# Kernel optimization log

Hardware: AMD Instinct MI355X
Metric: run time of the kernel (lower is better)

The kernel has to match this reference:

```python
import jax, jax.numpy as jnp
import numpy as np

E, B, S, C, N, D, DFF, H, K_FREQ = 4, 16, 256, 17, 16, 32, 64, 4, 4
DH = D // H
MA_KERNELS = (4, 8, 12)


def setup_inputs() -> dict:
    key = jax.random.key(0)
    ks = jax.random.split(key, 16)
    sc = 1.0 / np.sqrt(D).astype(np.float32)
    inp = {
        "x": jax.random.normal(ks[0], (B, S, C, 1), jnp.float32),
        "original_x": jax.random.uniform(ks[1], (B, S, 2), jnp.float32),
        "start_W": jax.random.normal(ks[2], (D,), jnp.float32),
        "start_b": jnp.zeros((D,), jnp.float32),
        "Wq": jax.random.normal(ks[3], (E, D, D), jnp.float32) * sc,
        "Wk": jax.random.normal(ks[4], (E, D, D), jnp.float32) * sc,
        "Wv": jax.random.normal(ks[5], (E, D, D), jnp.float32) * sc,
        "Wo": jax.random.normal(ks[6], (E, D, D), jnp.float32) * sc,
        "ln1_g": jnp.ones((E, D), jnp.float32),
        "ln1_b": jnp.zeros((E, D), jnp.float32),
        "ln2_g": jnp.ones((E, D), jnp.float32),
        "ln2_b": jnp.zeros((E, D), jnp.float32),
        "W1": jax.random.normal(ks[7], (E, D, DFF), jnp.float32) * sc,
        "b1": jnp.zeros((E, DFF), jnp.float32),
        "W2": jax.random.normal(ks[8], (E, DFF, D), jnp.float32) * (1.0 / np.sqrt(DFF).astype(np.float32)),
        "b2": jnp.zeros((E, D), jnp.float32),
    }
    return inp


def _moving_avg(x, k):
    # x: [B,S,Ch], replicate-pad then uniform window of size k (stride 1)
    front = jnp.repeat(x[:, :1], (k - 1) // 2, axis=1)
    end = jnp.repeat(x[:, -1:], k // 2, axis=1)
    xp = jnp.concatenate([front, x, end], axis=1)  # [B, S+k-1, Ch]
    c = jnp.cumsum(xp, axis=1)
    c = jnp.concatenate([jnp.zeros_like(c[:, :1]), c], axis=1)
    return (c[:, k:] - c[:, :-k]) / jnp.asarray(k, x.dtype)


def _fourier_season(x, k):
    # ETSformer-style FourierLayer: keep top-k amplitude frequencies (excluding DC)
    s = x.shape[1]
    xf = jnp.fft.rfft(x, axis=1)            # [B,F,Ch] complex
    amp = jnp.abs(xf)
    amp = amp.at[:, 0, :].set(-jnp.inf)     # exclude DC
    topv = jax.lax.top_k(jnp.moveaxis(amp, 1, -1), k)[0]  # [B,Ch,k]
    thresh = topv[..., -1]                  # [B,Ch]
    mask = amp >= thresh[:, None, :]
    xf_m = jnp.where(mask, xf, 0)
    return jnp.fft.irfft(xf_m, n=s, axis=1).astype(x.dtype)


def _ln(z, g, b):
    m = jnp.mean(z, -1, keepdims=True)
    v = jnp.var(z, -1, keepdims=True)
    return (z - m) * jax.lax.rsqrt(v + 1e-5) * g + b


def _expert_fwd(args):
    h, wq, wk, wv, wo, g1, bg1, g2, bg2, w1, b1e, w2, b2e = args
    # h: [B,S,N,D]; pre-LN MHA over the sequence axis per (batch, node)
    z = _ln(h, g1, bg1)
    q = jnp.einsum('bsnd,de->bsne', z, wq).reshape(B, S, N, H, DH)
    k_ = jnp.einsum('bsnd,de->bsne', z, wk).reshape(B, S, N, H, DH)
    v_ = jnp.einsum('bsnd,de->bsne', z, wv).reshape(B, S, N, H, DH)
    att = jnp.einsum('bqnhd,bknhd->bnhqk', q, k_) * (1.0 / np.sqrt(DH).astype(np.float32))
    att = jax.nn.softmax(att, axis=-1)
    o = jnp.einsum('bnhqk,bknhd->bqnhd', att, v_).reshape(B, S, N, D)
    h = h + jnp.einsum('bsnd,de->bsne', o, wo)
    z2 = _ln(h, g2, bg2)
    f = jax.nn.relu(jnp.einsum('bsnd,df->bsnf', z2, w1) + b1e)
    h = h + jnp.einsum('bsnf,fd->bsnd', f, w2) + b2e
    return h


def reference(x, original_x, start_W, start_b, Wq, Wk, Wv, Wo,
              ln1_g, ln1_b, ln2_g, ln2_b, W1, b1, W2, b2):
    xc = x[:, :, :, 0]                                  # [B,S,C]
    trend = sum(_moving_avg(xc, k) for k in MA_KERNELS) / float(len(MA_KERNELS))
    season = _fourier_season(xc, K_FREQ)
    new_x = xc + season + trend                         # [B,S,C]

    scores = original_x[:, :, -1]                       # [B,S]
    bins = jnp.linspace(scores.min(), scores.max(), E + 1)
    assign = jnp.clip(jnp.searchsorted(bins, scores, side='right') - 1, 0, E - 1)  # [B,S] int

    xns = new_x[:, :, :-1]                              # [B,S,N] drop score channel
    onehot = (assign[None] == jnp.arange(E)[:, None, None])          # [E,B,S] bool
    expert_in = xns[None] * onehot[..., None].astype(xns.dtype)      # [E,B,S,N] dense zero-padded dispatch
    hidden = expert_in[..., None] * start_W + start_b                # [E,B,S,N,D] start_linear

    outs = jax.lax.map(_expert_fwd, (hidden, Wq, Wk, Wv, Wo,
                                     ln1_g, ln1_b, ln2_g, ln2_b, W1, b1, W2, b2))  # [E,B,S,N,D]
    combined = jnp.einsum('ebs,ebsnd->bsnd', onehot.astype(outs.dtype), outs)      # one-hot combine
    return combined
```

## Files before the change

### kernel.cpp

```cpp
#include <hip/hip_runtime.h>
#include <hip/hip_fp16.h>
#include <math.h>

#define BB 16
#define SS 256
#define CC 17
#define NCH 16
#define DD 32
#define DFFN 64
#define HH 4
#define DH 8
#define EE 4

#define WS_K0 16
#define WS_V0 144
#define WS_XNS 512
#define WS_SPI (WS_XNS + BB*SS*NCH)
#define WS_WT  (WS_SPI + BB*SS + 64)
#define WS_WL  (WS_WT + 6144)

#define PRE 0.51006977f

typedef __fp16 hv2 __attribute__((ext_vector_type(2)));

__device__ __forceinline__ unsigned pkh2(float a, float b) {
  hv2 r = __builtin_amdgcn_cvt_pkrtz(a, b);
  unsigned u; __builtin_memcpy(&u, &r, 4);
  return u;
}
__device__ __forceinline__ float fd2(unsigned a, unsigned b, float c) {
  hv2 av, bv;
  __builtin_memcpy(&av, &a, 4);
  __builtin_memcpy(&bv, &b, 4);
  return __builtin_amdgcn_fdot2(av, bv, c, false);
}
__device__ __forceinline__ __half2 u2h2(unsigned u) {
  __half2 h; __builtin_memcpy(&h, &u, 4); return h;
}
template<int PAT>
__device__ __forceinline__ unsigned qdpp(unsigned v) {
  return (unsigned)__builtin_amdgcn_mov_dpp((int)v, PAT, 0xF, 0xF, true);
}
template<int PAT>
__device__ __forceinline__ float qdppf(float v) {
  return __uint_as_float(qdpp<PAT>(__float_as_uint(v)));
}

__launch_bounds__(1024)
__global__ void decomp_prep_kernel(const float* __restrict__ x,
                                   const float* __restrict__ ox,
                                   const float* __restrict__ sb,
                                   const float* __restrict__ g1,
                                   const float* __restrict__ bb1,
                                   const float* __restrict__ Wq,
                                   const float* __restrict__ Wk,
                                   const float* __restrict__ Wv,
                                   const float* __restrict__ Wo,
                                   const float* __restrict__ W1,
                                   const float* __restrict__ W2,
                                   float* __restrict__ ws) {
  const int t = threadIdx.x;
  if (blockIdx.x < 256) {
    const int b = blockIdx.x / NCH;
    const int c = blockIdx.x % NCH;
    __shared__ float xs[SS];
    __shared__ float prr[1024], pii[1024];
    __shared__ float amp[129];
    __shared__ float2 YY[129];
    __shared__ float sth;
    if (t < SS) xs[t] = x[(b*SS + t)*CC + c];
    __syncthreads();
    const float TH0 = 0.024543692606170259f;
    {
      const int f = (t & 127) + 1;
      const int chunk = t >> 7;
      const int s0 = chunk * 32;
      const int ph0 = (f * s0) & 255;
      float si, cr; sincosf(TH0*(float)ph0, &si, &cr);
      float s1, c1; sincosf(TH0*(float)f, &s1, &c1);
      float xr = 0.f, xi = 0.f;
      #pragma unroll 4
      for (int k = 0; k < 32; ++k) {
        float xvv = xs[s0 + k];
        xr += xvv * cr;
        xi -= xvv * si;
        float nc = cr*c1 - si*s1;
        si = si*c1 + cr*s1;
        cr = nc;
      }
      prr[t] = xr; pii[t] = xi;
    }
    __syncthreads();
    if (t < 128) {
      float xr = 0.f, xi = 0.f;
      #pragma unroll
      for (int k2 = 0; k2 < 8; ++k2) { xr += prr[t + 128*k2]; xi += pii[t + 128*k2]; }
      prr[t] = xr; pii[t] = xi;
      amp[t+1] = sqrtf(xr*xr + xi*xi);
    }
    __syncthreads();
    if (t < 64) {
      float a0 = amp[t+1], a1 = amp[t+65];
      int i0 = t+1, i1 = t+65;
      float th = -1e30f;
      for (int r = 0; r < 4; ++r) {
        float mv = (a0 > a1) ? a0 : a1;
        int   mi = (a0 > a1) ? i0 : i1;
        for (int off = 32; off > 0; off >>= 1) {
          float ov = __shfl_xor(mv, off);
          int   oi = __shfl_xor(mi, off);
          if (ov > mv || (ov == mv && oi < mi)) { mv = ov; mi = oi; }
        }
        th = mv;
        if (mi == i0) a0 = -1e30f;
        if (mi == i1) a1 = -1e30f;
      }
      if (t == 0) sth = th;
    }
    __syncthreads();
    if (t < 128) {
      const int f = t + 1;
      float wgt = (amp[f] >= sth) ? ((f == 128) ? 1.0f : 2.0f) * (1.0f/256.0f) : 0.0f;
      YY[f] = make_float2(wgt * prr[t], wgt * pii[t]);
    }
    __syncthreads();
    {
      const int s = t & 255;
      const int fc = t >> 8;
      const int f0 = 1 + fc*32;
      const int ph0 = (s * f0) & 255;
      float si, cr; sincosf(TH0*(float)ph0, &si, &cr);
      float s1, c1; sincosf(TH0*(float)s, &s1, &c1);
      float acc = 0.f;
      #pragma unroll 4
      for (int k = 0; k < 32; ++k) {
        float2 y = YY[f0 + k];
        acc += y.x*cr - y.y*si;
        float nc = cr*c1 - si*s1;
        si = si*c1 + cr*s1;
        cr = nc;
      }
      prr[t] = acc;
    }
    __syncthreads();
    if (t < 256) {
      float season = prr[t] + prr[t+256] + prr[t+512] + prr[t+768];
      float s4 = 0.f, s8 = 0.f, s12 = 0.f;
      #pragma unroll
      for (int j = 0; j < 4; ++j)  { int p = t + j - 1; p = p < 0 ? 0 : (p > SS-1 ? SS-1 : p); s4  += xs[p]; }
      #pragma unroll
      for (int j = 0; j < 8; ++j)  { int p = t + j - 3; p = p < 0 ? 0 : (p > SS-1 ? SS-1 : p); s8  += xs[p]; }
      #pragma unroll
      for (int j = 0; j < 12; ++j) { int p = t + j - 5; p = p < 0 ? 0 : (p > SS-1 ? SS-1 : p); s12 += xs[p]; }
      float trend = (s4 * 0.25f + s8 * 0.125f + s12 * (1.0f/12.0f)) * (1.0f/3.0f);
      ws[WS_XNS + (b*SS + t)*NCH + c] = xs[t] + season + trend;
    }
  } else if (blockIdx.x < 272) {
    const int b = blockIdx.x - 256;
    __shared__ float red[32];
    __shared__ int asg[SS];
    __shared__ int cnt[EE];
    __shared__ float z0[EE*DD];
    float mn = 3e38f, mx = -3e38f;
    #pragma unroll
    for (int k = 0; k < 4; ++k) {
      float v = ox[(t + k*1024)*2 + 1];
      mn = fminf(mn, v); mx = fmaxf(mx, v);
    }
    for (int off = 32; off > 0; off >>= 1) {
      mn = fminf(mn, __shfl_xor(mn, off));
      mx = fmaxf(mx, __shfl_xor(mx, off));
    }
    if ((t & 63) == 0) { red[(t>>6)*2] = mn; red[(t>>6)*2+1] = mx; }
    __syncthreads();
    mn = red[0]; mx = red[1];
    #pragma unroll
    for (int w = 1; w < 16; ++w) { mn = fminf(mn, red[w*2]); mx = fmaxf(mx, red[w*2+1]); }
    const float step = (mx - mn) * 0.25f;
    const float e1 = mn + step, e2 = mn + 2.f*step, e3 = mn + 3.f*step;
    if (t < 256) {
      float sc = ox[(b*SS + t)*2 + 1];
      asg[t] = (sc >= e1) + (sc >= e2) + (sc >= e3);
    }
    __syncthreads();
    if (t < EE) {
      int c = 0;
      for (int s2 = 0; s2 < SS; ++s2) c += (asg[s2] == t);
      cnt[t] = c;
    }
    __syncthreads();
    int* SPw  = (int*)ws + WS_SPI;
    int* OFFw = SPw + BB*SS;
    if (t < EE) {
      int off = 0;
      for (int i = 0; i < t; ++i) off += cnt[i];
      OFFw[b*EE + t] = off;
      int kp = off;
      for (int s2 = 0; s2 < SS; ++s2) if (asg[s2] == t) SPw[b*SS + (kp++)] = s2;
    }
    if (t < 128) {
      int ee = t >> 5, d = t & 31;
      float m = 0.f;
      for (int i = 0; i < DD; ++i) m += sb[i];
      m *= (1.0f/DD);
      float var = 0.f;
      for (int i = 0; i < DD; ++i) { float df = sb[i]-m; var += df*df; }
      var *= (1.0f/DD);
      float rs = rsqrtf(var + 1e-5f);
      z0[ee*DD + d] = (sb[d]-m)*rs*g1[ee*DD+d] + bb1[ee*DD+d];
    }
    __syncthreads();
    if (b == 0 && t < 128) {
      int ee = t >> 5, d = t & 31;
      float k0 = 0.f, v0 = 0.f;
      for (int i = 0; i < DD; ++i) {
        float zz = z0[ee*DD + i];
        k0 += zz * Wk[ee*DD*DD + i*DD + d];
        v0 += zz * Wv[ee*DD*DD + i*DD + d];
      }
      ws[WS_K0 + ee*DD + d] = k0;
      ws[WS_V0 + ee*DD + d] = v0;
    }
  } else {
    unsigned* img = (unsigned*)ws + WS_WT;
    const int base_u = (blockIdx.x - 272)*4096;
    #pragma unroll
    for (int i = 0; i < 4; ++i) {
      int u = base_u + i*1024 + t;
      unsigned val;
      if (u < 6144) {
        int mat = u >> 11, r = u & 2047;
        int row = r >> 4, ip = r & 15;
        int e = row >> 5, q = row & 31;
        int d = (q & 3)*8 + (q >> 2);
        const float* Wm = (mat == 0) ? Wq : (mat == 1) ? Wk : Wv;
        const float* src = Wm + e*1024 + d;
        val = pkh2(src[ip*64], src[ip*64 + 32]);
      } else {
        int v = u - 6144;
        if (v < 2048) {
          int row = v >> 4, ip = v & 15;
          int e = row >> 5, q = row & 31;
          int d = (q & 3)*8 + (q >> 2);
          const float* src = Wo + e*1024 + d;
          val = pkh2(src[ip*64], src[ip*64 + 32]);
        } else if (v < 6144) {
          int r = v - 2048;
          int row = r >> 4, ip = r & 15;
          int e = row >> 6, q = row & 63;
          int j = (q & 3)*16 + (q >> 2);
          const float* src = W1 + e*2048 + j;
          val = pkh2(src[ip*128], src[ip*128 + 64]);
        } else {
          int r = v - 6144;
          int a = r >> 11, rr = r & 2047;
          int row = rr >> 4, ip = rr & 15;
          int e = row >> 5, q = row & 31;
          int d = (q & 3)*8 + (q >> 2);
          int jp = a*16 + ip;
          const float* src = W2 + e*2048 + d;
          val = pkh2(src[2*jp*32], src[(2*jp+1)*32]);
        }
      }
      img[u] = val;
    }
  }
}

__launch_bounds__(1024, 4)
__global__ void fused_kernel(const float* __restrict__ ws,
    const float* __restrict__ g1, const float* __restrict__ bb1,
    const float* __restrict__ sW, const float* __restrict__ sb,
    const float* __restrict__ g2, const float* __restrict__ bb2,
    const float* __restrict__ b1, const float* __restrict__ b2,
    float* __restrict__ out) {
  const int blk = blockIdx.x;
  const int n = blk & 15;
  const int b = blk >> 4;
  const int t = threadIdx.x;
  const int p = t >> 2;
  const int hh = t & 3;
  __shared__ unsigned lds[24576];
  unsigned* wT = lds + 8192;
  unsigned* wl = lds + 14336;

  {
    const unsigned* img = (const unsigned*)ws + WS_WT;
    const int wv = t >> 6;
    const int ln = t & 63;
    #pragma unroll
    for (int i = 0; i < 4; ++i) {
      const int ch = wv*4 + i;
      __builtin_amdgcn_global_load_lds(
          (const __attribute__((address_space(1))) unsigned*)(img + ch*256 + ln*4),
          (__attribute__((address_space(3))) unsigned*)(wT + ch*256 + ln*4),
          16, 0, 0);
    }
  }

  const int* SP  = (const int*)ws + WS_SPI;
  const int* OFF = SP + BB*SS;
  const int o1 = OFF[b*4+1], o2v = OFF[b*4+2], o3 = OFF[b*4+3];
  const int e = (p >= o1) + (p >= o2v) + (p >= o3);
  const int beg = (e==0) ? 0  : ((e==1) ? o1 : ((e==2) ? o2v : o3));
  const int end = (e==0) ? o1 : ((e==1) ? o2v : ((e==2) ? o3 : SS));
  const int s = SP[b*SS + p];
  const float xv = ws[WS_XNS + (b*SS + s)*NCH + n];

  float h[DD];
  #pragma unroll
  for (int d = 0; d < DD; ++d) h[d] = xv * sW[d] + sb[d];
  float m = 0.f;
  #pragma unroll
  for (int d = 0; d < DD; ++d) m += h[d];
  m *= (1.0f/DD);
  float var = 0.f;
  #pragma unroll
  for (int d = 0; d < DD; ++d) { float df = h[d]-m; var += df*df; }
  var *= (1.0f/DD);
  float rs = rsqrtf(var + 1e-5f);
  unsigned zp[16];
  #pragma unroll
  for (int ip = 0; ip < 16; ++ip) {
    float za = (h[2*ip]  -m)*rs*g1[e*DD+2*ip]   + bb1[e*DD+2*ip];
    float zb = (h[2*ip+1]-m)*rs*g1[e*DD+2*ip+1] + bb1[e*DD+2*ip+1];
    zp[ip] = pkh2(za, zb);
  }
  __syncthreads();

  float q[DH], kk[DH], vv[DH];
  #pragma unroll
  for (int dd = 0; dd < DH; ++dd) {
    const int row16 = (e*32 + dd*4 + hh)*16;
    const uint4* rq = (const uint4*)&wT[row16];
    const uint4* rk = (const uint4*)&wT[2048 + row16];
    const uint4* rv = (const uint4*)&wT[4096 + row16];
    float aq = 0.f, ak = 0.f, av = 0.f;
    #pragma unroll
    for (int g4 = 0; g4 < 4; ++g4) {
      uint4 wq4 = rq[g4], wk4 = rk[g4], wv4 = rv[g4];
      aq = fd2(zp[4*g4+0], wq4.x, aq); aq = fd2(zp[4*g4+1], wq4.y, aq);
      aq = fd2(zp[4*g4+2], wq4.z, aq); aq = fd2(zp[4*g4+3], wq4.w, aq);
      ak = fd2(zp[4*g4+0], wk4.x, ak); ak = fd2(zp[4*g4+1], wk4.y, ak);
      ak = fd2(zp[4*g4+2], wk4.z, ak); ak = fd2(zp[4*g4+3], wk4.w, ak);
      av = fd2(zp[4*g4+0], wv4.x, av); av = fd2(zp[4*g4+1], wv4.y, av);
      av = fd2(zp[4*g4+2], wv4.z, av); av = fd2(zp[4*g4+3], wv4.w, av);
    }
    q[dd] = aq * PRE; kk[dd] = ak; vv[dd] = av;
  }
  *(uint4*)&lds[p*32 + hh*8]     = make_uint4(pkh2(kk[0],kk[1]), pkh2(kk[2],kk[3]),
                                              pkh2(kk[4],kk[5]), pkh2(kk[6],kk[7]));
  *(uint4*)&lds[p*32 + hh*8 + 4] = make_uint4(pkh2(vv[0],vv[1]), pkh2(vv[2],vv[3]),
                                              pkh2(vv[4],vv[5]), pkh2(vv[6],vv[7]));
  unsigned qp2[4];
  #pragma unroll
  for (int i = 0; i < 4; ++i) qp2[i] = pkh2(q[2*i], q[2*i+1]);
  float s0 = 0.f;
  #pragma unroll
  for (int d = 0; d < DH; ++d) s0 += q[d] * ws[WS_K0 + e*DD + hh*DH + d];
  __syncthreads();

  float wsum = 0.f;
  __half2 o2[4];
  #pragma unroll
  for (int i = 0; i < 4; ++i) o2[i] = u2h2(0u);
  int jk = beg;
  for (; jk + 1 < end; jk += 2) {
    uint4 ku0 = *(const uint4*)&lds[jk*32 + hh*8];
    uint4 vu0 = *(const uint4*)&lds[jk*32 + hh*8 + 4];
    uint4 ku1 = *(const uint4*)&lds[(jk+1)*32 + hh*8];
    uint4 vu1 = *(const uint4*)&lds[(jk+1)*32 + hh*8 + 4];
    float a0 = 0.f, a1 = 0.f;
    a0 = fd2(qp2[0], ku0.x, a0); a0 = fd2(qp2[1], ku0.y, a0);
    a0 = fd2(qp2[2], ku0.z, a0); a0 = fd2(qp2[3], ku0.w, a0);
    a1 = fd2(qp2[0], ku1.x, a1); a1 = fd2(qp2[1], ku1.y, a1);
    a1 = fd2(qp2[2], ku1.z, a1); a1 = fd2(qp2[3], ku1.w, a1);
    float w0f = __builtin_amdgcn_exp2f(a0);
    float w1f = __builtin_amdgcn_exp2f(a1);
    wsum += w0f + w1f;
    __half2 w20 = u2h2(pkh2(w0f, w0f));
    __half2 w21 = u2h2(pkh2(w1f, w1f));
    o2[0] = __hfma2(w20, u2h2(vu0.x), o2[0]);
    o2[1] = __hfma2(w20, u2h2(vu0.y), o2[1]);
    o2[2] = __hfma2(w20, u2h2(vu0.z), o2[2]);
    o2[3] = __hfma2(w20, u2h2(vu0.w), o2[3]);
    o2[0] = __hfma2(w21, u2h2(vu1.x), o2[0]);
    o2[1] = __hfma2(w21, u2h2(vu1.y), o2[1]);
    o2[2] = __hfma2(w21, u2h2(vu1.z), o2[2]);
    o2[3] = __hfma2(w21, u2h2(vu1.w), o2[3]);
  }
  if (jk < end) {
    uint4 ku = *(const uint4*)&lds[jk*32 + hh*8];
    uint4 vu = *(const uint4*)&lds[jk*32 + hh*8 + 4];
    float a = 0.f;
    a = fd2(qp2[0], ku.x, a); a = fd2(qp2[1], ku.y, a);
    a = fd2(qp2[2], ku.z, a); a = fd2(qp2[3], ku.w, a);
    float wf = __builtin_amdgcn_exp2f(a);
    wsum += wf;
    __half2 w2 = u2h2(pkh2(wf, wf));
    o2[0] = __hfma2(w2, u2h2(vu.x), o2[0]);
    o2[1] = __hfma2(w2, u2h2(vu.y), o2[1]);
    o2[2] = __hfma2(w2, u2h2(vu.z), o2[2]);
    o2[3] = __hfma2(w2, u2h2(vu.w), o2[3]);
  }
  float o[DH];
  #pragma unroll
  for (int i = 0; i < 4; ++i) {
    o[2*i]   = __low2float(o2[i]);
    o[2*i+1] = __high2float(o2[i]);
  }
  const int nmis = SS - (end - beg);
  float w0 = (float)nmis * __builtin_amdgcn_exp2f(s0);
  wsum += w0;
  #pragma unroll
  for (int d = 0; d < DH; ++d) o[d] += w0 * ws[WS_V0 + e*DD + hh*DH + d];
  float inv = 1.0f / wsum;
  #pragma unroll
  for (int d = 0; d < DH; ++d) o[d] *= inv;

  unsigned oq[4];
  #pragma unroll
  for (int j = 0; j < 4; ++j) oq[j] = pkh2(o[2*j], o[2*j+1]);
  unsigned ovp[16];
  #pragma unroll
  for (int j = 0; j < 4; ++j) {
    ovp[j]    = qdpp<0x00>(oq[j]);
    ovp[4+j]  = qdpp<0x55>(oq[j]);
    ovp[8+j]  = qdpp<0xAA>(oq[j]);
    ovp[12+j] = qdpp<0xFF>(oq[j]);
  }

  float acc[DH];
  #pragma unroll
  for (int dd = 0; dd < DH; ++dd) {
    int d = hh*DH + dd;
    const uint4* row = (const uint4*)&wl[(e*32 + dd*4 + hh)*16];
    float a = xv * sW[d] + sb[d];
    #pragma unroll
    for (int g4 = 0; g4 < 4; ++g4) {
      uint4 w4 = row[g4];
      a = fd2(ovp[4*g4+0], w4.x, a); a = fd2(ovp[4*g4+1], w4.y, a);
      a = fd2(ovp[4*g4+2], w4.z, a); a = fd2(ovp[4*g4+3], w4.w, a);
    }
    acc[dd] = a;
  }

  float ssum = 0.f;
  #pragma unroll
  for (int dd = 0; dd < DH; ++dd) ssum += acc[dd];
  ssum += qdppf<0xB1>(ssum);
  ssum += qdppf<0x4E>(ssum);
  float m2 = ssum * (1.0f/DD);
  float vs = 0.f;
  #pragma unroll
  for (int dd = 0; dd < DH; ++dd) { float df = acc[dd]-m2; vs += df*df; }
  vs += qdppf<0xB1>(vs);
  vs += qdppf<0x4E>(vs);
  float rs2 = rsqrtf(vs * (1.0f/DD) + 1e-5f);
  unsigned zq[4];
  #pragma unroll
  for (int j = 0; j < 4; ++j) {
    int d = hh*DH + 2*j;
    float za = (acc[2*j]  -m2)*rs2*g2[e*DD+d]   + bb2[e*DD+d];
    float zb = (acc[2*j+1]-m2)*rs2*g2[e*DD+d+1] + bb2[e*DD+d+1];
    zq[j] = pkh2(za, zb);
  }
  unsigned zp2[16];
  #pragma unroll
  for (int j = 0; j < 4; ++j) {
    zp2[j]    = qdpp<0x00>(zq[j]);
    zp2[4+j]  = qdpp<0x55>(zq[j]);
    zp2[8+j]  = qdpp<0xAA>(zq[j]);
    zp2[12+j] = qdpp<0xFF>(zq[j]);
  }

  float f[16];
  #pragma unroll
  for (int jj = 0; jj < 16; ++jj) {
    const uint4* row = (const uint4*)&wl[2048 + (e*64 + jj*4 + hh)*16];
    float a = b1[e*DFFN + hh*16 + jj];
    #pragma unroll
    for (int g4 = 0; g4 < 4; ++g4) {
      uint4 w4 = row[g4];
      a = fd2(zp2[4*g4+0], w4.x, a); a = fd2(zp2[4*g4+1], w4.y, a);
      a = fd2(zp2[4*g4+2], w4.z, a); a = fd2(zp2[4*g4+3], w4.w, a);
    }
    f[jj] = fmaxf(a, 0.0f);
  }
  unsigned fq[8];
  #pragma unroll
  for (int j = 0; j < 8; ++j) fq[j] = pkh2(f[2*j], f[2*j+1]);
  unsigned fu[32];
  #pragma unroll
  for (int j = 0; j < 8; ++j) {
    fu[j]    = qdpp<0x00>(fq[j]);
    fu[8+j]  = qdpp<0x55>(fq[j]);
    fu[16+j] = qdpp<0xAA>(fq[j]);
    fu[24+j] = qdpp<0xFF>(fq[j]);
  }

  float acc2[DH];
  #pragma unroll
  for (int dd = 0; dd < DH; ++dd) {
    int d = hh*DH + dd;
    const int row16 = (e*32 + dd*4 + hh)*16;
    float a = acc[dd] + b2[e*DD + d];
    #pragma unroll
    for (int g4 = 0; g4 < 8; ++g4) {
      const int plane = (g4 >> 2);
      uint4 w4 = *(const uint4*)&wl[6144 + plane*2048 + row16 + 4*(g4 & 3)];
      a = fd2(fu[4*g4+0], w4.x, a); a = fd2(fu[4*g4+1], w4.y, a);
      a = fd2(fu[4*g4+2], w4.z, a); a = fd2(fu[4*g4+3], w4.w, a);
    }
    acc2[dd] = a;
  }
  float* op = out + ((size_t)((b*SS + s)*NCH + n))*DD + hh*DH;
  *(float4*)(op)     = make_float4(acc2[0], acc2[1], acc2[2], acc2[3]);
  *(float4*)(op + 4) = make_float4(acc2[4], acc2[5], acc2[6], acc2[7]);
}

extern "C" void kernel_launch(void* const* d_in, const int* in_sizes, int n_in,
                              void* d_out, int out_size, void* d_ws, size_t ws_size,
                              hipStream_t stream) {
  (void)in_sizes; (void)n_in; (void)out_size; (void)ws_size;
  const float* x   = (const float*)d_in[0];
  const float* ox  = (const float*)d_in[1];
  const float* sW  = (const float*)d_in[2];
  const float* sb  = (const float*)d_in[3];
  const float* Wq  = (const float*)d_in[4];
  const float* Wk  = (const float*)d_in[5];
  const float* Wv  = (const float*)d_in[6];
  const float* Wo  = (const float*)d_in[7];
  const float* g1  = (const float*)d_in[8];
  const float* b1n = (const float*)d_in[9];
  const float* g2  = (const float*)d_in[10];
  const float* b2n = (const float*)d_in[11];
  const float* W1  = (const float*)d_in[12];
  const float* bf1 = (const float*)d_in[13];
  const float* W2  = (const float*)d_in[14];
  const float* bf2 = (const float*)d_in[15];
  float* out = (float*)d_out;
  float* ws  = (float*)d_ws;

  decomp_prep_kernel<<<276, 1024, 0, stream>>>(x, ox, sb, g1, b1n,
                                               Wq, Wk, Wv, Wo, W1, W2, ws);
  fused_kernel<<<BB*NCH, 1024, 0, stream>>>(ws, g1, b1n, sW, sb, g2, b2n,
                                            bf1, bf2, out);
}
```

Measured before the change: 134.9 us.

## Split attention keys across four query lanes with XOR-swizzled LDS K/V layout

```diff
diff --git a/kernel.cpp b/kernel.cpp
--- a/kernel.cpp
+++ b/kernel.cpp
@@ -36,6 +36,12 @@
 }
 __device__ __forceinline__ __half2 u2h2(unsigned u) {
   __half2 h; __builtin_memcpy(&h, &u, 4); return h;
+}
+__device__ __forceinline__ __half2 shx_h2(__half2 x, int m) {
+  int v; __builtin_memcpy(&v, &x, 4);
+  v = __shfl_xor(v, m);
+  __half2 r; __builtin_memcpy(&r, &v, 4);
+  return r;
 }
 template<int PAT>
 __device__ __forceinline__ unsigned qdpp(unsigned v) {
@@ -348,72 +354,118 @@
     }
     q[dd] = aq * PRE; kk[dd] = ak; vv[dd] = av;
   }
-  *(uint4*)&lds[p*32 + hh*8]     = make_uint4(pkh2(kk[0],kk[1]), pkh2(kk[2],kk[3]),
-                                              pkh2(kk[4],kk[5]), pkh2(kk[6],kk[7]));
-  *(uint4*)&lds[p*32 + hh*8 + 4] = make_uint4(pkh2(vv[0],vv[1]), pkh2(vv[2],vv[3]),
-                                              pkh2(vv[4],vv[5]), pkh2(vv[6],vv[7]));
+  const int kwidx = (p*32 + hh*8) ^ ((p & 7) << 2);
+  *(uint4*)&lds[kwidx]     = make_uint4(pkh2(kk[0],kk[1]), pkh2(kk[2],kk[3]),
+                                        pkh2(kk[4],kk[5]), pkh2(kk[6],kk[7]));
+  *(uint4*)&lds[kwidx ^ 4] = make_uint4(pkh2(vv[0],vv[1]), pkh2(vv[2],vv[3]),
+                                        pkh2(vv[4],vv[5]), pkh2(vv[6],vv[7]));
   unsigned qp2[4];
   #pragma unroll
   for (int i = 0; i < 4; ++i) qp2[i] = pkh2(q[2*i], q[2*i+1]);
+  unsigned qx1[4], qx2[4], qx3[4];
+  #pragma unroll
+  for (int i = 0; i < 4; ++i) {
+    qx1[i] = (unsigned)__shfl_xor((int)qp2[i], 4);
+    qx2[i] = (unsigned)__shfl_xor((int)qp2[i], 8);
+    qx3[i] = (unsigned)__shfl_xor((int)qp2[i], 12);
+  }
   float s0 = 0.f;
   #pragma unroll
   for (int d = 0; d < DH; ++d) s0 += q[d] * ws[WS_K0 + e*DD + hh*DH + d];
   __syncthreads();
 
-  float wsum = 0.f;
-  __half2 o2[4];
-  #pragma unroll
-  for (int i = 0; i < 4; ++i) o2[i] = u2h2(0u);
-  int jk = beg;
-  for (; jk + 1 < end; jk += 2) {
-    uint4 ku0 = *(const uint4*)&lds[jk*32 + hh*8];
-    uint4 vu0 = *(const uint4*)&lds[jk*32 + hh*8 + 4];
-    uint4 ku1 = *(const uint4*)&lds[(jk+1)*32 + hh*8];
-    uint4 vu1 = *(const uint4*)&lds[(jk+1)*32 + hh*8 + 4];
-    float a0 = 0.f, a1 = 0.f;
-    a0 = fd2(qp2[0], ku0.x, a0); a0 = fd2(qp2[1], ku0.y, a0);
-    a0 = fd2(qp2[2], ku0.z, a0); a0 = fd2(qp2[3], ku0.w, a0);
-    a1 = fd2(qp2[0], ku1.x, a1); a1 = fd2(qp2[1], ku1.y, a1);
-    a1 = fd2(qp2[2], ku1.z, a1); a1 = fd2(qp2[3], ku1.w, a1);
-    float w0f = __builtin_amdgcn_exp2f(a0);
-    float w1f = __builtin_amdgcn_exp2f(a1);
-    wsum += w0f + w1f;
-    __half2 w20 = u2h2(pkh2(w0f, w0f));
-    __half2 w21 = u2h2(pkh2(w1f, w1f));
-    o2[0] = __hfma2(w20, u2h2(vu0.x), o2[0]);
-    o2[1] = __hfma2(w20, u2h2(vu0.y), o2[1]);
-    o2[2] = __hfma2(w20, u2h2(vu0.z), o2[2]);
-    o2[3] = __hfma2(w20, u2h2(vu0.w), o2[3]);
-    o2[0] = __hfma2(w21, u2h2(vu1.x), o2[0]);
-    o2[1] = __hfma2(w21, u2h2(vu1.y), o2[1]);
-    o2[2] = __hfma2(w21, u2h2(vu1.z), o2[2]);
-    o2[3] = __hfma2(w21, u2h2(vu1.w), o2[3]);
-  }
-  if (jk < end) {
-    uint4 ku = *(const uint4*)&lds[jk*32 + hh*8];
-    uint4 vu = *(const uint4*)&lds[jk*32 + hh*8 + 4];
-    float a = 0.f;
-    a = fd2(qp2[0], ku.x, a); a = fd2(qp2[1], ku.y, a);
-    a = fd2(qp2[2], ku.z, a); a = fd2(qp2[3], ku.w, a);
-    float wf = __builtin_amdgcn_exp2f(a);
-    wsum += wf;
-    __half2 w2 = u2h2(pkh2(wf, wf));
-    o2[0] = __hfma2(w2, u2h2(vu.x), o2[0]);
-    o2[1] = __hfma2(w2, u2h2(vu.y), o2[1]);
-    o2[2] = __hfma2(w2, u2h2(vu.z), o2[2]);
-    o2[3] = __hfma2(w2, u2h2(vu.w), o2[3]);
+  const int sl = p & 3;
+  const int gb = p & ~3;
+  const int egA = (gb     >= o1) + (gb     >= o2v) + (gb     >= o3);
+  const int egB = ((gb+3) >= o1) + ((gb+3) >= o2v) + ((gb+3) >= o3);
+
+  float ws0 = 0.f, ws1 = 0.f, ws2 = 0.f, ws3 = 0.f;
+  __half2 oa0[4], oa1[4], oa2[4], oa3[4];
+  #pragma unroll
+  for (int j = 0; j < 4; ++j) {
+    oa0[j] = u2h2(0u); oa1[j] = u2h2(0u);
+    oa2[j] = u2h2(0u); oa3[j] = u2h2(0u);
+  }
+
+  if (egA == egB) {
+    for (int jk = beg + sl; jk < end; jk += 4) {
+      const int kidx = (jk*32 + hh*8) ^ ((jk & 7) << 2);
+      const uint4 ku = *(const uint4*)&lds[kidx];
+      const uint4 vu = *(const uint4*)&lds[kidx ^ 4];
+      float a0 = 0.f, a1 = 0.f, a2 = 0.f, a3 = 0.f;
+      a0 = fd2(qp2[0], ku.x, a0); a0 = fd2(qp2[1], ku.y, a0);
+      a0 = fd2(qp2[2], ku.z, a0); a0 = fd2(qp2[3], ku.w, a0);
+      a1 = fd2(qx1[0], ku.x, a1); a1 = fd2(qx1[1], ku.y, a1);
+      a1 = fd2(qx1[2], ku.z, a1); a1 = fd2(qx1[3], ku.w, a1);
+      a2 = fd2(qx2[0], ku.x, a2); a2 = fd2(qx2[1], ku.y, a2);
+      a2 = fd2(qx2[2], ku.z, a2); a2 = fd2(qx2[3], ku.w, a2);
+      a3 = fd2(qx3[0], ku.x, a3); a3 = fd2(qx3[1], ku.y, a3);
+      a3 = fd2(qx3[2], ku.z, a3); a3 = fd2(qx3[3], ku.w, a3);
+      const float w0 = __builtin_amdgcn_exp2f(a0);
+      const float w1 = __builtin_amdgcn_exp2f(a1);
+      const float w2 = __builtin_amdgcn_exp2f(a2);
+      const float w3 = __builtin_amdgcn_exp2f(a3);
+      ws0 += w0; ws1 += w1; ws2 += w2; ws3 += w3;
+      const __half2 hw0 = u2h2(pkh2(w0, w0));
+      const __half2 hw1 = u2h2(pkh2(w1, w1));
+      const __half2 hw2 = u2h2(pkh2(w2, w2));
+      const __half2 hw3 = u2h2(pkh2(w3, w3));
+      oa0[0] = __hfma2(hw0, u2h2(vu.x), oa0[0]);
+      oa0[1] = __hfma2(hw0, u2h2(vu.y), oa0[1]);
+      oa0[2] = __hfma2(hw0, u2h2(vu.z), oa0[2]);
+      oa0[3] = __hfma2(hw0, u2h2(vu.w), oa0[3]);
+      oa1[0] = __hfma2(hw1, u2h2(vu.x), oa1[0]);
+      oa1[1] = __hfma2(hw1, u2h2(vu.y), oa1[1]);
+      oa1[2] = __hfma2(hw1, u2h2(vu.z), oa1[2]);
+      oa1[3] = __hfma2(hw1, u2h2(vu.w), oa1[3]);
+      oa2[0] = __hfma2(hw2, u2h2(vu.x), oa2[0]);
+      oa2[1] = __hfma2(hw2, u2h2(vu.y), oa2[1]);
+      oa2[2] = __hfma2(hw2, u2h2(vu.z), oa2[2]);
+      oa2[3] = __hfma2(hw2, u2h2(vu.w), oa2[3]);
+      oa3[0] = __hfma2(hw3, u2h2(vu.x), oa3[0]);
+      oa3[1] = __hfma2(hw3, u2h2(vu.y), oa3[1]);
+      oa3[2] = __hfma2(hw3, u2h2(vu.z), oa3[2]);
+      oa3[3] = __hfma2(hw3, u2h2(vu.w), oa3[3]);
+    }
+  } else {
+    for (int jk = beg; jk < end; ++jk) {
+      const int kidx = (jk*32 + hh*8) ^ ((jk & 7) << 2);
+      const uint4 ku = *(const uint4*)&lds[kidx];
+      const uint4 vu = *(const uint4*)&lds[kidx ^ 4];
+      float a0 = 0.f;
+      a0 = fd2(qp2[0], ku.x, a0); a0 = fd2(qp2[1], ku.y, a0);
+      a0 = fd2(qp2[2], ku.z, a0); a0 = fd2(qp2[3], ku.w, a0);
+      const float w0 = __builtin_amdgcn_exp2f(a0);
+      ws0 += w0;
+      const __half2 hw0 = u2h2(pkh2(w0, w0));
+      oa0[0] = __hfma2(hw0, u2h2(vu.x), oa0[0]);
+      oa0[1] = __hfma2(hw0, u2h2(vu.y), oa0[1]);
+      oa0[2] = __hfma2(hw0, u2h2(vu.z), oa0[2]);
+      oa0[3] = __hfma2(hw0, u2h2(vu.w), oa0[3]);
+    }
+  }
+
+  float wsum;
+  {
+    const float wA = ws0 + __shfl_xor(ws1, 4);
+    const float wB = ws2 + __shfl_xor(ws3, 4);
+    wsum = wA + __shfl_xor(wB, 8);
   }
   float o[DH];
   #pragma unroll
-  for (int i = 0; i < 4; ++i) {
-    o[2*i]   = __low2float(o2[i]);
-    o[2*i+1] = __high2float(o2[i]);
-  }
+  for (int j = 0; j < 4; ++j) {
+    const __half2 oA = __hadd2(oa0[j], shx_h2(oa1[j], 4));
+    const __half2 oB = __hadd2(oa2[j], shx_h2(oa3[j], 4));
+    const __half2 of = __hadd2(oA, shx_h2(oB, 8));
+    o[2*j]   = __low2float(of);
+    o[2*j+1] = __high2float(of);
+  }
+
   const int nmis = SS - (end - beg);
-  float w0 = (float)nmis * __builtin_amdgcn_exp2f(s0);
-  wsum += w0;
-  #pragma unroll
-  for (int d = 0; d < DH; ++d) o[d] += w0 * ws[WS_V0 + e*DD + hh*DH + d];
+  float w0c = (float)nmis * __builtin_amdgcn_exp2f(s0);
+  wsum += w0c;
+  #pragma unroll
+  for (int d = 0; d < DH; ++d) o[d] += w0c * ws[WS_V0 + e*DD + hh*DH + d];
   float inv = 1.0f / wsum;
   #pragma unroll
   for (int d = 0; d < DH; ++d) o[d] *= inv;
```

Measured after the change: 141.7 us. 5.1% more time.

## Fold start_linear and LayerNorm1 into closed-form QKV projection coefficients

Applied to the files above, without the earlier changes.

```diff
diff --git a/kernel.cpp b/kernel.cpp
--- a/kernel.cpp
+++ b/kernel.cpp
@@ -17,7 +17,6 @@
 #define WS_XNS 512
 #define WS_SPI (WS_XNS + BB*SS*NCH)
 #define WS_WT  (WS_SPI + BB*SS + 64)
-#define WS_WL  (WS_WT + 6144)
 
 #define PRE 0.51006977f
 
@@ -49,6 +48,7 @@
 __launch_bounds__(1024)
 __global__ void decomp_prep_kernel(const float* __restrict__ x,
                                    const float* __restrict__ ox,
+                                   const float* __restrict__ sW,
                                    const float* __restrict__ sb,
                                    const float* __restrict__ g1,
                                    const float* __restrict__ bb1,
@@ -221,48 +221,75 @@
       ws[WS_K0 + ee*DD + d] = k0;
       ws[WS_V0 + ee*DD + d] = v0;
     }
-  } else {
+  } else if (blockIdx.x < 275) {
     unsigned* img = (unsigned*)ws + WS_WT;
     const int base_u = (blockIdx.x - 272)*4096;
     #pragma unroll
     for (int i = 0; i < 4; ++i) {
       int u = base_u + i*1024 + t;
-      unsigned val;
-      if (u < 6144) {
-        int mat = u >> 11, r = u & 2047;
-        int row = r >> 4, ip = r & 15;
-        int e = row >> 5, q = row & 31;
-        int d = (q & 3)*8 + (q >> 2);
-        const float* Wm = (mat == 0) ? Wq : (mat == 1) ? Wk : Wv;
-        const float* src = Wm + e*1024 + d;
-        val = pkh2(src[ip*64], src[ip*64 + 32]);
-      } else {
-        int v = u - 6144;
-        if (v < 2048) {
-          int row = v >> 4, ip = v & 15;
-          int e = row >> 5, q = row & 31;
-          int d = (q & 3)*8 + (q >> 2);
+      if (u < 10240) {
+        unsigned val;
+        if (u < 2048) {
+          int row = u >> 4, ip = u & 15;
+          int e = row >> 5, qq = row & 31;
+          int d = (qq & 3)*8 + (qq >> 2);
           const float* src = Wo + e*1024 + d;
           val = pkh2(src[ip*64], src[ip*64 + 32]);
-        } else if (v < 6144) {
-          int r = v - 2048;
+        } else if (u < 6144) {
+          int r = u - 2048;
           int row = r >> 4, ip = r & 15;
-          int e = row >> 6, q = row & 63;
-          int j = (q & 3)*16 + (q >> 2);
+          int e = row >> 6, qq = row & 63;
+          int j = (qq & 3)*16 + (qq >> 2);
           const float* src = W1 + e*2048 + j;
           val = pkh2(src[ip*128], src[ip*128 + 64]);
         } else {
-          int r = v - 6144;
+          int r = u - 6144;
           int a = r >> 11, rr = r & 2047;
           int row = rr >> 4, ip = rr & 15;
-          int e = row >> 5, q = row & 31;
-          int d = (q & 3)*8 + (q >> 2);
+          int e = row >> 5, qq = row & 31;
+          int d = (qq & 3)*8 + (qq >> 2);
           int jp = a*16 + ip;
           const float* src = W2 + e*2048 + d;
           val = pkh2(src[2*jp*32], src[(2*jp+1)*32]);
         }
-      }
-      img[u] = val;
+        img[u] = val;
+      }
+    }
+  } else {
+    __shared__ float s_a[DD], s_c[DD];
+    if (t < DD) { s_a[t] = sW[t]; s_c[t] = sb[t]; }
+    __syncthreads();
+    if (t == 0) {
+      float mW = 0.f, mb = 0.f;
+      for (int d = 0; d < DD; ++d) { mW += s_a[d]; mb += s_c[d]; }
+      mW *= (1.0f/DD); mb *= (1.0f/DD);
+      float A = 0.f, Bv = 0.f, Cv = 0.f;
+      for (int d = 0; d < DD; ++d) {
+        float a = s_a[d] - mW, c = s_c[d] - mb;
+        s_a[d] = a; s_c[d] = c;
+        A += a*a; Bv += a*c; Cv += c*c;
+      }
+      ws[8]  = A  * (1.0f/DD);
+      ws[9]  = Bv * (1.0f/DD);
+      ws[10] = Cv * (1.0f/DD);
+    }
+    __syncthreads();
+    if (t < 384) {
+      const int m = t >> 7, r = t & 127, e = r >> 5, j = r & 31;
+      const float* Wm = (m == 0) ? Wq : (m == 1) ? Wk : Wv;
+      float pp = 0.f, qq = 0.f, rr = 0.f;
+      for (int d = 0; d < DD; ++d) {
+        float w  = Wm[e*DD*DD + d*DD + j];
+        float gg = g1[e*DD + d];
+        pp += s_a[d]*gg*w;
+        qq += s_c[d]*gg*w;
+        rr += bb1[e*DD + d]*w;
+      }
+      float* pqr = ws + WS_WT + 10240;
+      const int base = (m*EE + e)*96 + j;
+      pqr[base]      = pp;
+      pqr[base + 32] = qq;
+      pqr[base + 64] = rr;
     }
   }
 }
@@ -280,20 +307,19 @@
   const int t = threadIdx.x;
   const int p = t >> 2;
   const int hh = t & 3;
-  __shared__ unsigned lds[24576];
-  unsigned* wT = lds + 8192;
-  unsigned* wl = lds + 14336;
+  __shared__ unsigned lds[20480];
+  unsigned* wl = lds + 8192;
 
   {
     const unsigned* img = (const unsigned*)ws + WS_WT;
     const int wv = t >> 6;
     const int ln = t & 63;
     #pragma unroll
-    for (int i = 0; i < 4; ++i) {
-      const int ch = wv*4 + i;
+    for (int i = 0; i < 3; ++i) {
+      const int ch = wv*3 + i;
       __builtin_amdgcn_global_load_lds(
           (const __attribute__((address_space(1))) unsigned*)(img + ch*256 + ln*4),
-          (__attribute__((address_space(3))) unsigned*)(wT + ch*256 + ln*4),
+          (__attribute__((address_space(3))) unsigned*)(wl + ch*256 + ln*4),
           16, 0, 0);
     }
   }
@@ -307,47 +333,36 @@
   const int s = SP[b*SS + p];
   const float xv = ws[WS_XNS + (b*SS + s)*NCH + n];
 
-  float h[DD];
-  #pragma unroll
-  for (int d = 0; d < DD; ++d) h[d] = xv * sW[d] + sb[d];
-  float m = 0.f;
-  #pragma unroll
-  for (int d = 0; d < DD; ++d) m += h[d];
-  m *= (1.0f/DD);
-  float var = 0.f;
-  #pragma unroll
-  for (int d = 0; d < DD; ++d) { float df = h[d]-m; var += df*df; }
-  var *= (1.0f/DD);
-  float rs = rsqrtf(var + 1e-5f);
-  unsigned zp[16];
-  #pragma unroll
-  for (int ip = 0; ip < 16; ++ip) {
-    float za = (h[2*ip]  -m)*rs*g1[e*DD+2*ip]   + bb1[e*DD+2*ip];
-    float zb = (h[2*ip+1]-m)*rs*g1[e*DD+2*ip+1] + bb1[e*DD+2*ip+1];
-    zp[ip] = pkh2(za, zb);
-  }
+  const float Ac = ws[8], Bc = ws[9], Cc = ws[10];
+  const float var = fmaf(xv, fmaf(Ac, xv, Bc + Bc), Cc);
+  const float rs = rsqrtf(var + 1e-5f);
+  const float alpha = rs * xv, beta = rs;
   __syncthreads();
 
+  const float* pqr = (const float*)(wl + 10240);
   float q[DH], kk[DH], vv[DH];
   #pragma unroll
-  for (int dd = 0; dd < DH; ++dd) {
-    const int row16 = (e*32 + dd*4 + hh)*16;
-    const uint4* rq = (const uint4*)&wT[row16];
-    const uint4* rk = (const uint4*)&wT[2048 + row16];
-    const uint4* rv = (const uint4*)&wT[4096 + row16];
-    float aq = 0.f, ak = 0.f, av = 0.f;
-    #pragma unroll
-    for (int g4 = 0; g4 < 4; ++g4) {
-      uint4 wq4 = rq[g4], wk4 = rk[g4], wv4 = rv[g4];
-      aq = fd2(zp[4*g4+0], wq4.x, aq); aq = fd2(zp[4*g4+1], wq4.y, aq);
-      aq = fd2(zp[4*g4+2], wq4.z, aq); aq = fd2(zp[4*g4+3], wq4.w, aq);
-      ak = fd2(zp[4*g4+0], wk4.x, ak); ak = fd2(zp[4*g4+1], wk4.y, ak);
-      ak = fd2(zp[4*g4+2], wk4.z, ak); ak = fd2(zp[4*g4+3], wk4.w, ak);
-      av = fd2(zp[4*g4+0], wv4.x, av); av = fd2(zp[4*g4+1], wv4.y, av);
-      av = fd2(zp[4*g4+2], wv4.z, av); av = fd2(zp[4*g4+3], wv4.w, av);
-    }
-    q[dd] = aq * PRE; kk[dd] = ak; vv[dd] = av;
-  }
+  for (int m = 0; m < 3; ++m) {
+    const float* bp = &pqr[(m*EE + e)*96 + hh*DH];
+    const float4 P0 = *(const float4*)(bp);
+    const float4 P1 = *(const float4*)(bp + 4);
+    const float4 Q0 = *(const float4*)(bp + 32);
+    const float4 Q1 = *(const float4*)(bp + 36);
+    const float4 R0 = *(const float4*)(bp + 64);
+    const float4 R1 = *(const float4*)(bp + 68);
+    float* dst = (m == 0) ? q : (m == 1) ? kk : vv;
+    dst[0] = fmaf(alpha, P0.x, fmaf(beta, Q0.x, R0.x));
+    dst[1] = fmaf(alpha, P0.y, fmaf(beta, Q0.y, R0.y));
+    dst[2] = fmaf(alpha, P0.z, fmaf(beta, Q0.z, R0.z));
+    dst[3] = fmaf(alpha, P0.w, fmaf(beta, Q0.w, R0.w));
+    dst[4] = fmaf(alpha, P1.x, fmaf(beta, Q1.x, R1.x));
+    dst[5] = fmaf(alpha, P1.y, fmaf(beta, Q1.y, R1.y));
+    dst[6] = fmaf(alpha, P1.z, fmaf(beta, Q1.z, R1.z));
+    dst[7] = fmaf(alpha, P1.w, fmaf(beta, Q1.w, R1.w));
+  }
+  #pragma unroll
+  for (int dd = 0; dd < DH; ++dd) q[dd] *= PRE;
+
   *(uint4*)&lds[p*32 + hh*8]     = make_uint4(pkh2(kk[0],kk[1]), pkh2(kk[2],kk[3]),
                                               pkh2(kk[4],kk[5]), pkh2(kk[6],kk[7]));
   *(uint4*)&lds[p*32 + hh*8 + 4] = make_uint4(pkh2(vv[0],vv[1]), pkh2(vv[2],vv[3]),
@@ -542,7 +557,7 @@
   float* out = (float*)d_out;
   float* ws  = (float*)d_ws;
 
-  decomp_prep_kernel<<<276, 1024, 0, stream>>>(x, ox, sb, g1, b1n,
+  decomp_prep_kernel<<<276, 1024, 0, stream>>>(x, ox, sW, sb, g1, b1n,
                                                Wq, Wk, Wv, Wo, W1, W2, ws);
   fused_kernel<<<BB*NCH, 1024, 0, stream>>>(ws, g1, b1n, sW, sb, g2, b2n,
                                             bf1, bf2, out);
```

Result: no change. 135.6 us (+0.5%).
